# Kernel tuning notes

Hardware: AMD Instinct MI355X
Metric: run time of the kernel (lower is better)

Reference implementation:

```python
import jax, jax.numpy as jnp
import numpy as np

L, B, T = 512, 4096, 25

def setup_inputs() -> dict:
    key = jax.random.key(0)
    k = jax.random.split(key, 5)
    return {
        "emissions": jax.random.normal(k[0], (L, B, T), dtype=jnp.float32),
        "tags": jax.random.randint(k[1], (L, B), 0, T),
        "transitions": jax.random.normal(k[2], (T, T), dtype=jnp.float32) * 0.1,
        "start_transitions": jax.random.normal(k[3], (T,), dtype=jnp.float32) * 0.1,
        "end_transitions": jax.random.normal(k[4], (T,), dtype=jnp.float32) * 0.1,
    }


def _crf_nll(emissions, tags, transitions, start_transitions, end_transitions):
    # emissions: [L,B,T], tags: [L,B] int. Full mask (all timesteps valid).
    b = jnp.arange(emissions.shape[1])
    # ---- numerator: score of the gold path ----
    first = start_transitions[tags[0]] + emissions[0, b, tags[0]]  # [B]

    def num_step(carry, inp):
        prev_tags, score = carry
        em_t, tg_t = inp
        score = score + transitions[prev_tags, tg_t] + em_t[b, tg_t]
        return (tg_t, score), None

    (last_tags, numerator), _ = jax.lax.scan(
        num_step, (tags[0], first), (emissions[1:], tags[1:]))
    numerator = numerator + end_transitions[last_tags]
    # ---- denominator: log partition via forward algorithm ----
    alpha0 = start_transitions[None, :] + emissions[0]  # [B,T]

    def fwd_step(alpha, em_t):
        # alpha: [B,T] (prev tag), transitions: [T_prev, T_next]
        nxt = jax.nn.logsumexp(alpha[:, :, None] + transitions[None, :, :], axis=1) + em_t
        return nxt, None

    alpha, _ = jax.lax.scan(fwd_step, alpha0, emissions[1:])
    log_z = jax.nn.logsumexp(alpha + end_transitions[None, :], axis=1)  # [B]
    # reduction='mean' over batch of log-likelihood, negated
    return -jnp.mean(numerator - log_z)


def _crf_decode(emissions, transitions, start_transitions, end_transitions):
    # Viterbi over [L,B,T] with full mask.
    b = jnp.arange(emissions.shape[1])
    score0 = start_transitions[None, :] + emissions[0]  # [B,T]

    def vit_step(score, em_t):
        # total: [B, T_prev, T_next]
        total = score[:, :, None] + transitions[None, :, :] + em_t[:, None, :]
        best_prev = jnp.argmax(total, axis=1).astype(jnp.int32)  # [B,T]
        return jnp.max(total, axis=1), best_prev

    score, history = jax.lax.scan(vit_step, score0, emissions[1:])  # history [L-1,B,T]
    last_tag = jnp.argmax(score + end_transitions[None, :], axis=1).astype(jnp.int32)  # [B]

    def back_step(nxt_tag, hist_t):
        prev_tag = hist_t[b, nxt_tag]  # [B]
        return prev_tag, prev_tag

    _, prev_tags = jax.lax.scan(back_step, last_tag, history, reverse=True)  # [L-1,B]
    return jnp.concatenate([prev_tags, last_tag[None, :]], axis=0)  # [L,B]


def reference(emissions, tags, transitions, start_transitions, end_transitions):
    nll = _crf_nll(emissions, tags, transitions, start_transitions, end_transitions)
    best_path = _crf_decode(emissions, transitions, start_transitions, end_transitions)
    return nll, best_path
```

## Files before the change

### kernel.cpp

```cpp
#include <hip/hip_runtime.h>

#define TN 25
#define BN 4096
#define LN 512
#define NEG_INF (-__builtin_huge_valf())

__device__ __forceinline__ float gmax32(float x) {
  x = fmaxf(x, __int_as_float(__builtin_amdgcn_ds_swizzle(__float_as_int(x), 0x041F)));
  x = fmaxf(x, __int_as_float(__builtin_amdgcn_ds_swizzle(__float_as_int(x), 0x081F)));
  x = fmaxf(x, __int_as_float(__builtin_amdgcn_ds_swizzle(__float_as_int(x), 0x101F)));
  x = fmaxf(x, __int_as_float(__builtin_amdgcn_ds_swizzle(__float_as_int(x), 0x201F)));
  x = fmaxf(x, __int_as_float(__builtin_amdgcn_ds_swizzle(__float_as_int(x), 0x401F)));
  return x;
}
__device__ __forceinline__ float gsum32(float x) {
  x = x + __int_as_float(__builtin_amdgcn_ds_swizzle(__float_as_int(x), 0x041F));
  x = x + __int_as_float(__builtin_amdgcn_ds_swizzle(__float_as_int(x), 0x081F));
  x = x + __int_as_float(__builtin_amdgcn_ds_swizzle(__float_as_int(x), 0x101F));
  x = x + __int_as_float(__builtin_amdgcn_ds_swizzle(__float_as_int(x), 0x201F));
  x = x + __int_as_float(__builtin_amdgcn_ds_swizzle(__float_as_int(x), 0x401F));
  return x;
}

template <int P>
__device__ __forceinline__ void vit_cand(int sci, const float (&tc)[TN], float em,
                                         float (&v)[TN]) {
  v[P] = (__int_as_float(__builtin_amdgcn_ds_swizzle(sci, (P << 5))) + tc[P]) + em;
  if constexpr (P + 1 < TN) vit_cand<P + 1>(sci, tc, em, v);
}

template <int P>
__device__ __forceinline__ void fwd_acc(int eai, const float (&ec)[TN], float& s0, float& s1) {
  float ep = __int_as_float(__builtin_amdgcn_ds_swizzle(eai, (P << 5)));
  if constexpr ((P & 1) == 0) { s0 = fmaf(ep, ec[P], s0); } else { s1 = fmaf(ep, ec[P], s1); }
  if constexpr (P + 1 < TN) fwd_acc<P + 1>(eai, ec, s0, s1);
}

__global__ __launch_bounds__(512, 4) void crf_main(
    const float* __restrict__ emis, const int* __restrict__ tags,
    const float* __restrict__ trans, const float* __restrict__ startT,
    const float* __restrict__ endT, float* __restrict__ nll_out,
    unsigned char* __restrict__ hist, unsigned char* __restrict__ mmap,
    int* __restrict__ lastTagOut) {
  __shared__ float ltr[TN * TN];
  const int tid = threadIdx.x;
  for (int i = tid; i < TN * TN; i += 512) ltr[i] = trans[i];
  __syncthreads();

  const int j = tid & 31;
  const int grp = tid >> 5;
  const int b = blockIdx.x * 8 + (grp & 7);
  const bool act = (j < TN);
  const int jj = act ? j : 0;
  const float endv = act ? endT[j] : NEG_INF;
  const float* emp = emis + (size_t)b * TN;
  const float em0 = act ? emp[j] : 0.0f;
  const float startv = act ? startT[j] : NEG_INF;

  if (grp < 8) {
    float tc[TN];
#pragma unroll
    for (int p = 0; p < TN; ++p) tc[p] = ltr[p * TN + jj];

    float score = startv + em0;
    int M = j;
    const int bp_base = (tid & 32) << 2;
    unsigned char* hp = hist + ((size_t)BN + b) * 32 + j;

#pragma unroll 1
    for (int t = 1; t < LN; ++t) {
      emp += (size_t)BN * TN;
      float em = act ? emp[j] : 0.0f;

      float v[TN];
      vit_cand<0>(__float_as_int(score), tc, em, v);

      int ix[TN];
#pragma unroll
      for (int p = 0; p < TN; ++p) ix[p] = p;
#pragma unroll
      for (int s = 1; s < TN; s <<= 1) {
#pragma unroll
        for (int i = 0; i + s < TN; i += 2 * s) {
          bool g = v[i + s] > v[i];
          v[i] = g ? v[i + s] : v[i];
          ix[i] = g ? ix[i + s] : ix[i];
        }
      }
      score = v[0];
      int barg = ix[0];

      if (act) *hp = (unsigned char)barg;
      hp += (size_t)BN * 32;

      M = __builtin_amdgcn_ds_bpermute(bp_base + (barg << 2), M);
      if ((t & 31) == 0) {
        int c = (t >> 5) - 1;
        if (act) mmap[((size_t)c * BN + b) * 32 + j] = (unsigned char)M;
        M = j;
      }
    }
    if (act) mmap[((size_t)15 * BN + b) * 32 + j] = (unsigned char)M;

    float vv = score + endv;
    float mv = gmax32(vv);
    unsigned long long bal = __ballot(vv == mv);
    unsigned int gb = (unsigned int)(bal >> (tid & 32));
    int lt = __ffs(gb) - 1;
    if (j == 0) lastTagOut[b] = lt;
  } else {
    float ec[TN];
#pragma unroll
    for (int p = 0; p < TN; ++p) ec[p] = __expf(ltr[p * TN + jj]);

    int tag = tags[b];
    float alpha = startv + em0;
    float num_acc = (j == tag) ? alpha : 0.0f;
    int ptag = tag;

#pragma unroll 1
    for (int t = 1; t < LN; ++t) {
      emp += (size_t)BN * TN;
      float em = act ? emp[j] : 0.0f;
      int tg = tags[(size_t)t * BN + b];

      float mA = __int_as_float(__builtin_amdgcn_ds_swizzle(__float_as_int(alpha), 0x0000));
      float ea = __expf(alpha - mA);

      float s0 = 0.0f, s1 = 0.0f;
      fwd_acc<0>(__float_as_int(ea), ec, s0, s1);
      alpha = act ? (__logf(s0 + s1) + mA + em) : NEG_INF;

      float trc = ltr[ptag * TN + jj];
      num_acc += (j == tg) ? (trc + em) : 0.0f;
      ptag = tg;
    }

    num_acc += (j == ptag) ? endv : 0.0f;
    float numerator = gsum32(num_acc);

    float va = alpha + endv;
    float m2 = gmax32(va);
    float ssum = gsum32(__expf(va - m2));
    float logZ = __logf(ssum) + m2;

    if (j == 0) atomicAdd(nll_out, (logZ - numerator) * (1.0f / BN));
  }
}

__global__ void crf_bstate(const unsigned char* __restrict__ mmap,
                           const int* __restrict__ lastTag,
                           int* __restrict__ estate) {
  int b = blockIdx.x * 256 + threadIdx.x;
  if (b >= BN) return;
  int s = lastTag[b];
  estate[15 * BN + b] = s;
#pragma unroll
  for (int c = 15; c >= 1; --c) {
    s = mmap[((size_t)c * BN + b) * 32 + s];
    estate[(c - 1) * BN + b] = s;
  }
}

__global__ void crf_backtrack(const unsigned char* __restrict__ hist,
                              const int* __restrict__ estate,
                              float* __restrict__ path) {
  int b = blockIdx.x * 256 + threadIdx.x;
  int c = blockIdx.y;
  int s = estate[c * BN + b];
  int te = (c == 15) ? (LN - 1) : 32 * (c + 1);
  for (int t = te; t > 32 * c; --t) {
    path[(size_t)t * BN + b] = (float)s;
    s = hist[((size_t)t * BN + b) * 32 + s];
  }
  if (c == 0) path[b] = (float)s;
}

extern "C" void kernel_launch(void* const* d_in, const int* in_sizes, int n_in,
                              void* d_out, int out_size, void* d_ws, size_t ws_size,
                              hipStream_t stream) {
  const float* emis   = (const float*)d_in[0];
  const int*   tags   = (const int*)d_in[1];
  const float* trans  = (const float*)d_in[2];
  const float* startT = (const float*)d_in[3];
  const float* endT   = (const float*)d_in[4];
  float* out = (float*)d_out;

  unsigned char* hist = (unsigned char*)d_ws;
  unsigned char* mmap = hist + (size_t)LN * BN * 32;
  int* lastTag = (int*)(mmap + (size_t)16 * BN * 32);
  int* estate  = lastTag + BN;

  hipMemsetAsync(d_out, 0, sizeof(float), stream);

  crf_main<<<dim3(BN / 8), 512, 0, stream>>>(emis, tags, trans, startT, endT,
                                             out, hist, mmap, lastTag);
  crf_bstate<<<dim3(BN / 256), 256, 0, stream>>>(mmap, lastTag, estate);
  crf_backtrack<<<dim3(BN / 256, 16), 256, 0, stream>>>(hist, estate, out + 1);
}
```

Baseline: 678.2 us.

## Split each CRF batch row across a full wave with LDS-broadcast recurrences

```diff
diff --git a/kernel.cpp b/kernel.cpp
--- a/kernel.cpp
+++ b/kernel.cpp
@@ -5,66 +5,73 @@
 #define LN 512
 #define NEG_INF (-__builtin_huge_valf())
 
+#define SWZF(x, imm) __int_as_float(__builtin_amdgcn_ds_swizzle(__float_as_int(x), (imm)))
+#define SWZI(x, imm) __builtin_amdgcn_ds_swizzle((x), (imm))
+
 __device__ __forceinline__ float gmax32(float x) {
-  x = fmaxf(x, __int_as_float(__builtin_amdgcn_ds_swizzle(__float_as_int(x), 0x041F)));
-  x = fmaxf(x, __int_as_float(__builtin_amdgcn_ds_swizzle(__float_as_int(x), 0x081F)));
-  x = fmaxf(x, __int_as_float(__builtin_amdgcn_ds_swizzle(__float_as_int(x), 0x101F)));
-  x = fmaxf(x, __int_as_float(__builtin_amdgcn_ds_swizzle(__float_as_int(x), 0x201F)));
-  x = fmaxf(x, __int_as_float(__builtin_amdgcn_ds_swizzle(__float_as_int(x), 0x401F)));
+  x = fmaxf(x, SWZF(x, 0x041F));
+  x = fmaxf(x, SWZF(x, 0x081F));
+  x = fmaxf(x, SWZF(x, 0x101F));
+  x = fmaxf(x, SWZF(x, 0x201F));
+  x = fmaxf(x, SWZF(x, 0x401F));
   return x;
 }
 __device__ __forceinline__ float gsum32(float x) {
-  x = x + __int_as_float(__builtin_amdgcn_ds_swizzle(__float_as_int(x), 0x041F));
-  x = x + __int_as_float(__builtin_amdgcn_ds_swizzle(__float_as_int(x), 0x081F));
-  x = x + __int_as_float(__builtin_amdgcn_ds_swizzle(__float_as_int(x), 0x101F));
-  x = x + __int_as_float(__builtin_amdgcn_ds_swizzle(__float_as_int(x), 0x201F));
-  x = x + __int_as_float(__builtin_amdgcn_ds_swizzle(__float_as_int(x), 0x401F));
+  x = x + SWZF(x, 0x041F);
+  x = x + SWZF(x, 0x081F);
+  x = x + SWZF(x, 0x101F);
+  x = x + SWZF(x, 0x201F);
+  x = x + SWZF(x, 0x401F);
   return x;
 }
 
-template <int P>
-__device__ __forceinline__ void vit_cand(int sci, const float (&tc)[TN], float em,
-                                         float (&v)[TN]) {
-  v[P] = (__int_as_float(__builtin_amdgcn_ds_swizzle(sci, (P << 5))) + tc[P]) + em;
-  if constexpr (P + 1 < TN) vit_cand<P + 1>(sci, tc, em, v);
-}
-
-template <int P>
-__device__ __forceinline__ void fwd_acc(int eai, const float (&ec)[TN], float& s0, float& s1) {
-  float ep = __int_as_float(__builtin_amdgcn_ds_swizzle(eai, (P << 5)));
-  if constexpr ((P & 1) == 0) { s0 = fmaf(ep, ec[P], s0); } else { s1 = fmaf(ep, ec[P], s1); }
-  if constexpr (P + 1 < TN) fwd_acc<P + 1>(eai, ec, s0, s1);
-}
-
-__global__ __launch_bounds__(512, 4) void crf_main(
+__global__ __launch_bounds__(512, 8) void crf_main(
     const float* __restrict__ emis, const int* __restrict__ tags,
     const float* __restrict__ trans, const float* __restrict__ startT,
     const float* __restrict__ endT, float* __restrict__ nll_out,
     unsigned char* __restrict__ hist, unsigned char* __restrict__ mmap,
     int* __restrict__ lastTagOut) {
   __shared__ float ltr[TN * TN];
+  __shared__ float ltrT[TN][36];
+  __shared__ float sv[8][32];
+
   const int tid = threadIdx.x;
-  for (int i = tid; i < TN * TN; i += 512) ltr[i] = trans[i];
+  for (int i = tid; i < TN * TN; i += 512) {
+    float v = trans[i];
+    ltr[i] = v;
+    ltrT[i % TN][i / TN] = v;
+  }
   __syncthreads();
 
-  const int j = tid & 31;
-  const int grp = tid >> 5;
-  const int b = blockIdx.x * 8 + (grp & 7);
+  const int wave = tid >> 6;
+  const int lane = tid & 63;
+  const int h = lane >> 5;
+  const int j = lane & 31;
+  const int b = blockIdx.x * 4 + (wave & 3);
   const bool act = (j < TN);
   const int jj = act ? j : 0;
+  const int pbase = h ? 12 : 0;
   const float endv = act ? endT[j] : NEG_INF;
   const float* emp = emis + (size_t)b * TN;
   const float em0 = act ? emp[j] : 0.0f;
   const float startv = act ? startT[j] : NEG_INF;
-
-  if (grp < 8) {
-    float tc[TN];
-#pragma unroll
-    for (int p = 0; p < TN; ++p) tc[p] = ltr[p * TN + jj];
-
+  float* svp = sv[wave];
+
+  float tcv[13];
+  {
+    const float4 a = *(const float4*)&ltrT[jj][pbase];
+    const float4 c = *(const float4*)&ltrT[jj][pbase + 4];
+    const float4 d = *(const float4*)&ltrT[jj][pbase + 8];
+    tcv[0] = a.x; tcv[1] = a.y; tcv[2] = a.z; tcv[3] = a.w;
+    tcv[4] = c.x; tcv[5] = c.y; tcv[6] = c.z; tcv[7] = c.w;
+    tcv[8] = d.x; tcv[9] = d.y; tcv[10] = d.z; tcv[11] = d.w;
+    tcv[12] = h ? ltrT[jj][24] : NEG_INF;
+  }
+
+  if (wave < 4) {
     float score = startv + em0;
+    if (h == 0 && act) svp[j] = score;
     int M = j;
-    const int bp_base = (tid & 32) << 2;
     unsigned char* hp = hist + ((size_t)BN + b) * 32 + j;
 
 #pragma unroll 1
@@ -72,51 +79,67 @@
       emp += (size_t)BN * TN;
       float em = act ? emp[j] : 0.0f;
 
-      float v[TN];
-      vit_cand<0>(__float_as_int(score), tc, em, v);
-
-      int ix[TN];
-#pragma unroll
-      for (int p = 0; p < TN; ++p) ix[p] = p;
-#pragma unroll
-      for (int s = 1; s < TN; s <<= 1) {
-#pragma unroll
-        for (int i = 0; i + s < TN; i += 2 * s) {
-          bool g = v[i + s] > v[i];
-          v[i] = g ? v[i + s] : v[i];
-          ix[i] = g ? ix[i + s] : ix[i];
+      const float4 a = *(const float4*)&svp[pbase];
+      const float4 c = *(const float4*)&svp[pbase + 4];
+      const float4 d = *(const float4*)&svp[pbase + 8];
+      const float sp12 = svp[pbase + 12];
+
+      float v[13]; int ix[13];
+      v[0] = (a.x + tcv[0]) + em;  v[1] = (a.y + tcv[1]) + em;
+      v[2] = (a.z + tcv[2]) + em;  v[3] = (a.w + tcv[3]) + em;
+      v[4] = (c.x + tcv[4]) + em;  v[5] = (c.y + tcv[5]) + em;
+      v[6] = (c.z + tcv[6]) + em;  v[7] = (c.w + tcv[7]) + em;
+      v[8] = (d.x + tcv[8]) + em;  v[9] = (d.y + tcv[9]) + em;
+      v[10] = (d.z + tcv[10]) + em; v[11] = (d.w + tcv[11]) + em;
+      v[12] = (sp12 + tcv[12]) + em;
+#pragma unroll
+      for (int k = 0; k < 13; ++k) ix[k] = pbase + k;
+
+#pragma unroll
+      for (int s = 1; s < 13; s <<= 1) {
+#pragma unroll
+        for (int i2 = 0; i2 + s < 13; i2 += 2 * s) {
+          bool g = v[i2 + s] > v[i2];
+          v[i2] = g ? v[i2 + s] : v[i2];
+          ix[i2] = g ? ix[i2 + s] : ix[i2];
         }
       }
-      score = v[0];
-      int barg = ix[0];
-
-      if (act) *hp = (unsigned char)barg;
+
+      float vo = SWZF(v[0], 0x401F);
+      int go = SWZI(ix[0], 0x401F);
+      float vh1 = h ? v[0] : vo, vh0 = h ? vo : v[0];
+      int gh1 = h ? ix[0] : go, gh0 = h ? go : ix[0];
+      bool better = vh1 > vh0;
+      score = better ? vh1 : vh0;
+      int barg = better ? gh1 : gh0;
+
+      if (h == 0 && act) svp[j] = score;
+      if (h == 0 && act) *hp = (unsigned char)barg;
       hp += (size_t)BN * 32;
 
-      M = __builtin_amdgcn_ds_bpermute(bp_base + (barg << 2), M);
+      M = __builtin_amdgcn_ds_bpermute((barg & 31) << 2, M);
       if ((t & 31) == 0) {
-        int c = (t >> 5) - 1;
-        if (act) mmap[((size_t)c * BN + b) * 32 + j] = (unsigned char)M;
+        int c2 = (t >> 5) - 1;
+        if (h == 0 && act) mmap[((size_t)c2 * BN + b) * 32 + j] = (unsigned char)M;
         M = j;
       }
     }
-    if (act) mmap[((size_t)15 * BN + b) * 32 + j] = (unsigned char)M;
+    if (h == 0 && act) mmap[((size_t)15 * BN + b) * 32 + j] = (unsigned char)M;
 
     float vv = score + endv;
     float mv = gmax32(vv);
     unsigned long long bal = __ballot(vv == mv);
-    unsigned int gb = (unsigned int)(bal >> (tid & 32));
+    unsigned int gb = (unsigned int)(bal >> (lane & 32));
     int lt = __ffs(gb) - 1;
-    if (j == 0) lastTagOut[b] = lt;
+    if (lane == 0) lastTagOut[b] = lt;
   } else {
-    float ec[TN];
-#pragma unroll
-    for (int p = 0; p < TN; ++p) ec[p] = __expf(ltr[p * TN + jj]);
-
-    int tag = tags[b];
+    float ecv[13];
+#pragma unroll
+    for (int k = 0; k < 13; ++k) ecv[k] = __expf(tcv[k]);
+
+    int ptag = tags[b];
     float alpha = startv + em0;
-    float num_acc = (j == tag) ? alpha : 0.0f;
-    int ptag = tag;
+    float num_acc = (act && j == ptag) ? alpha : 0.0f;
 
 #pragma unroll 1
     for (int t = 1; t < LN; ++t) {
@@ -124,19 +147,34 @@
       float em = act ? emp[j] : 0.0f;
       int tg = tags[(size_t)t * BN + b];
 
-      float mA = __int_as_float(__builtin_amdgcn_ds_swizzle(__float_as_int(alpha), 0x0000));
+      float mA = SWZF(alpha, 0x0000);
       float ea = __expf(alpha - mA);
-
-      float s0 = 0.0f, s1 = 0.0f;
-      fwd_acc<0>(__float_as_int(ea), ec, s0, s1);
-      alpha = act ? (__logf(s0 + s1) + mA + em) : NEG_INF;
+      if (h == 0 && act) svp[j] = ea;
+
+      const float4 a = *(const float4*)&svp[pbase];
+      const float4 c = *(const float4*)&svp[pbase + 4];
+      const float4 d = *(const float4*)&svp[pbase + 8];
+      const float ep12 = svp[pbase + 12];
+
+      float s0 = a.x * ecv[0];
+      float s1 = a.y * ecv[1];
+      s0 = fmaf(a.z, ecv[2], s0);  s1 = fmaf(a.w, ecv[3], s1);
+      s0 = fmaf(c.x, ecv[4], s0);  s1 = fmaf(c.y, ecv[5], s1);
+      s0 = fmaf(c.z, ecv[6], s0);  s1 = fmaf(c.w, ecv[7], s1);
+      s0 = fmaf(d.x, ecv[8], s0);  s1 = fmaf(d.y, ecv[9], s1);
+      s0 = fmaf(d.z, ecv[10], s0); s1 = fmaf(d.w, ecv[11], s1);
+      s0 = fmaf(ep12, ecv[12], s0);
+      float s = s0 + s1;
+      float tot = s + SWZF(s, 0x401F);
+
+      alpha = act ? (__logf(tot) + mA + em) : NEG_INF;
 
       float trc = ltr[ptag * TN + jj];
-      num_acc += (j == tg) ? (trc + em) : 0.0f;
+      num_acc += (act && j == tg) ? (trc + em) : 0.0f;
       ptag = tg;
     }
 
-    num_acc += (j == ptag) ? endv : 0.0f;
+    num_acc += (act && j == ptag) ? endv : 0.0f;
     float numerator = gsum32(num_acc);
 
     float va = alpha + endv;
@@ -144,7 +182,7 @@
     float ssum = gsum32(__expf(va - m2));
     float logZ = __logf(ssum) + m2;
 
-    if (j == 0) atomicAdd(nll_out, (logZ - numerator) * (1.0f / BN));
+    if (lane == 0) atomicAdd(nll_out, (logZ - numerator) * (1.0f / BN));
   }
 }
 
@@ -193,7 +231,7 @@
 
   hipMemsetAsync(d_out, 0, sizeof(float), stream);
 
-  crf_main<<<dim3(BN / 8), 512, 0, stream>>>(emis, tags, trans, startT, endT,
+  crf_main<<<dim3(BN / 4), 512, 0, stream>>>(emis, tags, trans, startT, endT,
                                              out, hist, mmap, lastTag);
   crf_bstate<<<dim3(BN / 256), 256, 0, stream>>>(mmap, lastTag, estate);
   crf_backtrack<<<dim3(BN / 256, 16), 256, 0, stream>>>(hist, estate, out + 1);
```

Result: no change. 678.5 us (+0.1%).

## Broadcast states via LDS vector reads and split Viterbi/forward into separate blocks

Applied to the files above, without the earlier changes.

```diff
diff --git a/kernel.cpp b/kernel.cpp
--- a/kernel.cpp
+++ b/kernel.cpp
@@ -3,66 +3,89 @@
 #define TN 25
 #define BN 4096
 #define LN 512
+#define NVB 512
 #define NEG_INF (-__builtin_huge_valf())
 
+#define SWZF(x, imm) __int_as_float(__builtin_amdgcn_ds_swizzle(__float_as_int(x), (imm)))
+
 __device__ __forceinline__ float gmax32(float x) {
-  x = fmaxf(x, __int_as_float(__builtin_amdgcn_ds_swizzle(__float_as_int(x), 0x041F)));
-  x = fmaxf(x, __int_as_float(__builtin_amdgcn_ds_swizzle(__float_as_int(x), 0x081F)));
-  x = fmaxf(x, __int_as_float(__builtin_amdgcn_ds_swizzle(__float_as_int(x), 0x101F)));
-  x = fmaxf(x, __int_as_float(__builtin_amdgcn_ds_swizzle(__float_as_int(x), 0x201F)));
-  x = fmaxf(x, __int_as_float(__builtin_amdgcn_ds_swizzle(__float_as_int(x), 0x401F)));
+  x = fmaxf(x, SWZF(x, 0x041F));
+  x = fmaxf(x, SWZF(x, 0x081F));
+  x = fmaxf(x, SWZF(x, 0x101F));
+  x = fmaxf(x, SWZF(x, 0x201F));
+  x = fmaxf(x, SWZF(x, 0x401F));
   return x;
 }
 __device__ __forceinline__ float gsum32(float x) {
-  x = x + __int_as_float(__builtin_amdgcn_ds_swizzle(__float_as_int(x), 0x041F));
-  x = x + __int_as_float(__builtin_amdgcn_ds_swizzle(__float_as_int(x), 0x081F));
-  x = x + __int_as_float(__builtin_amdgcn_ds_swizzle(__float_as_int(x), 0x101F));
-  x = x + __int_as_float(__builtin_amdgcn_ds_swizzle(__float_as_int(x), 0x201F));
-  x = x + __int_as_float(__builtin_amdgcn_ds_swizzle(__float_as_int(x), 0x401F));
+  x = x + SWZF(x, 0x041F);
+  x = x + SWZF(x, 0x081F);
+  x = x + SWZF(x, 0x101F);
+  x = x + SWZF(x, 0x201F);
+  x = x + SWZF(x, 0x401F);
   return x;
 }
 
-template <int P>
-__device__ __forceinline__ void vit_cand(int sci, const float (&tc)[TN], float em,
-                                         float (&v)[TN]) {
-  v[P] = (__int_as_float(__builtin_amdgcn_ds_swizzle(sci, (P << 5))) + tc[P]) + em;
-  if constexpr (P + 1 < TN) vit_cand<P + 1>(sci, tc, em, v);
-}
-
-template <int P>
-__device__ __forceinline__ void fwd_acc(int eai, const float (&ec)[TN], float& s0, float& s1) {
-  float ep = __int_as_float(__builtin_amdgcn_ds_swizzle(eai, (P << 5)));
-  if constexpr ((P & 1) == 0) { s0 = fmaf(ep, ec[P], s0); } else { s1 = fmaf(ep, ec[P], s1); }
-  if constexpr (P + 1 < TN) fwd_acc<P + 1>(eai, ec, s0, s1);
-}
-
-__global__ __launch_bounds__(512, 4) void crf_main(
+__device__ __forceinline__ void read_vec25(const float* __restrict__ p, float (&o)[TN]) {
+  const float4 q0 = *(const float4*)(p + 0);
+  const float4 q1 = *(const float4*)(p + 4);
+  const float4 q2 = *(const float4*)(p + 8);
+  const float4 q3 = *(const float4*)(p + 12);
+  const float4 q4 = *(const float4*)(p + 16);
+  const float4 q5 = *(const float4*)(p + 20);
+  o[0]=q0.x;  o[1]=q0.y;  o[2]=q0.z;  o[3]=q0.w;
+  o[4]=q1.x;  o[5]=q1.y;  o[6]=q1.z;  o[7]=q1.w;
+  o[8]=q2.x;  o[9]=q2.y;  o[10]=q2.z; o[11]=q2.w;
+  o[12]=q3.x; o[13]=q3.y; o[14]=q3.z; o[15]=q3.w;
+  o[16]=q4.x; o[17]=q4.y; o[18]=q4.z; o[19]=q4.w;
+  o[20]=q5.x; o[21]=q5.y; o[22]=q5.z; o[23]=q5.w;
+  o[24]=p[24];
+}
+
+__device__ __forceinline__ void merge3(float va, int ia, float vb, int ib, float vc, int ic,
+                                       float& mo, int& io) {
+  float m = fmaxf(fmaxf(va, vb), vc);
+  io = (m == va) ? ia : ((m == vb) ? ib : ic);
+  mo = m;
+}
+
+__global__ __launch_bounds__(256, 8) void crf_main(
     const float* __restrict__ emis, const int* __restrict__ tags,
     const float* __restrict__ trans, const float* __restrict__ startT,
     const float* __restrict__ endT, float* __restrict__ nll_out,
     unsigned char* __restrict__ hist, unsigned char* __restrict__ mmap,
     int* __restrict__ lastTagOut) {
   __shared__ float ltr[TN * TN];
+  __shared__ float ltrT[TN][28];
+  __shared__ float eltrT[TN][28];
+  __shared__ float sv[8][32];
+
   const int tid = threadIdx.x;
-  for (int i = tid; i < TN * TN; i += 512) ltr[i] = trans[i];
+  for (int i = tid; i < TN * TN; i += 256) {
+    float v = trans[i];
+    ltr[i] = v;
+    ltrT[i % TN][i / TN] = v;
+    eltrT[i % TN][i / TN] = __expf(v);
+  }
   __syncthreads();
 
   const int j = tid & 31;
   const int grp = tid >> 5;
-  const int b = blockIdx.x * 8 + (grp & 7);
   const bool act = (j < TN);
   const int jj = act ? j : 0;
   const float endv = act ? endT[j] : NEG_INF;
-  const float* emp = emis + (size_t)b * TN;
-  const float em0 = act ? emp[j] : 0.0f;
-  const float startv = act ? startT[j] : NEG_INF;
-
-  if (grp < 8) {
+  float* svp = sv[grp];
+
+  if (blockIdx.x < NVB) {
+    const int b = blockIdx.x * 8 + grp;
+    const float* emp = emis + (size_t)b * TN;
+    const float em0 = act ? emp[j] : 0.0f;
+    const float startv = act ? startT[j] : NEG_INF;
+
     float tc[TN];
-#pragma unroll
-    for (int p = 0; p < TN; ++p) tc[p] = ltr[p * TN + jj];
+    read_vec25(&ltrT[jj][0], tc);
 
     float score = startv + em0;
+    if (act) svp[j] = score;
     int M = j;
     const int bp_base = (tid & 32) << 2;
     unsigned char* hp = hist + ((size_t)BN + b) * 32 + j;
@@ -72,31 +95,35 @@
       emp += (size_t)BN * TN;
       float em = act ? emp[j] : 0.0f;
 
+      float sp[TN];
+      read_vec25(svp, sp);
+
       float v[TN];
-      vit_cand<0>(__float_as_int(score), tc, em, v);
-
-      int ix[TN];
-#pragma unroll
-      for (int p = 0; p < TN; ++p) ix[p] = p;
-#pragma unroll
-      for (int s = 1; s < TN; s <<= 1) {
-#pragma unroll
-        for (int i = 0; i + s < TN; i += 2 * s) {
-          bool g = v[i + s] > v[i];
-          v[i] = g ? v[i + s] : v[i];
-          ix[i] = g ? ix[i + s] : ix[i];
-        }
-      }
-      score = v[0];
-      int barg = ix[0];
-
+#pragma unroll
+      for (int p = 0; p < TN; ++p) v[p] = sp[p] + tc[p];
+
+      float w[9]; int wi[9];
+#pragma unroll
+      for (int g = 0; g < 8; ++g)
+        merge3(v[3*g], 3*g, v[3*g+1], 3*g+1, v[3*g+2], 3*g+2, w[g], wi[g]);
+      w[8] = v[24]; wi[8] = 24;
+      float u0, u1, u2; int x0, x1, x2;
+      merge3(w[0], wi[0], w[1], wi[1], w[2], wi[2], u0, x0);
+      merge3(w[3], wi[3], w[4], wi[4], w[5], wi[5], u1, x1);
+      merge3(w[6], wi[6], w[7], wi[7], w[8], wi[8], u2, x2);
+      float best; int barg;
+      merge3(u0, x0, u1, x1, u2, x2, best, barg);
+
+      score = best + em;
+
+      if (act) svp[j] = score;
       if (act) *hp = (unsigned char)barg;
       hp += (size_t)BN * 32;
 
       M = __builtin_amdgcn_ds_bpermute(bp_base + (barg << 2), M);
       if ((t & 31) == 0) {
-        int c = (t >> 5) - 1;
-        if (act) mmap[((size_t)c * BN + b) * 32 + j] = (unsigned char)M;
+        int c2 = (t >> 5) - 1;
+        if (act) mmap[((size_t)c2 * BN + b) * 32 + j] = (unsigned char)M;
         M = j;
       }
     }
@@ -109,14 +136,17 @@
     int lt = __ffs(gb) - 1;
     if (j == 0) lastTagOut[b] = lt;
   } else {
+    const int b = (blockIdx.x - NVB) * 8 + grp;
+    const float* emp = emis + (size_t)b * TN;
+    const float em0 = act ? emp[j] : 0.0f;
+    const float startv = act ? startT[j] : NEG_INF;
+
     float ec[TN];
-#pragma unroll
-    for (int p = 0; p < TN; ++p) ec[p] = __expf(ltr[p * TN + jj]);
-
-    int tag = tags[b];
+    read_vec25(&eltrT[jj][0], ec);
+
+    int ptag = tags[b];
     float alpha = startv + em0;
-    float num_acc = (j == tag) ? alpha : 0.0f;
-    int ptag = tag;
+    float num_acc = (act && j == ptag) ? alpha : 0.0f;
 
 #pragma unroll 1
     for (int t = 1; t < LN; ++t) {
@@ -124,19 +154,27 @@
       float em = act ? emp[j] : 0.0f;
       int tg = tags[(size_t)t * BN + b];
 
-      float mA = __int_as_float(__builtin_amdgcn_ds_swizzle(__float_as_int(alpha), 0x0000));
+      float mA = SWZF(alpha, 0x0000);
       float ea = __expf(alpha - mA);
-
-      float s0 = 0.0f, s1 = 0.0f;
-      fwd_acc<0>(__float_as_int(ea), ec, s0, s1);
+      if (act) svp[j] = ea;
+
+      float ep[TN];
+      read_vec25(svp, ep);
+
+      float s0 = ep[0] * ec[0];
+      float s1 = ep[1] * ec[1];
+#pragma unroll
+      for (int p = 2; p < TN; p += 2) s0 = fmaf(ep[p], ec[p], s0);
+#pragma unroll
+      for (int p = 3; p < TN; p += 2) s1 = fmaf(ep[p], ec[p], s1);
       alpha = act ? (__logf(s0 + s1) + mA + em) : NEG_INF;
 
       float trc = ltr[ptag * TN + jj];
-      num_acc += (j == tg) ? (trc + em) : 0.0f;
+      num_acc += (act && j == tg) ? (trc + em) : 0.0f;
       ptag = tg;
     }
 
-    num_acc += (j == ptag) ? endv : 0.0f;
+    num_acc += (act && j == ptag) ? endv : 0.0f;
     float numerator = gsum32(num_acc);
 
     float va = alpha + endv;
@@ -193,8 +231,8 @@
 
   hipMemsetAsync(d_out, 0, sizeof(float), stream);
 
-  crf_main<<<dim3(BN / 8), 512, 0, stream>>>(emis, tags, trans, startT, endT,
-                                             out, hist, mmap, lastTag);
+  crf_main<<<dim3(2 * NVB), 256, 0, stream>>>(emis, tags, trans, startT, endT,
+                                              out, hist, mmap, lastTag);
   crf_bstate<<<dim3(BN / 256), 256, 0, stream>>>(mmap, lastTag, estate);
   crf_backtrack<<<dim3(BN / 256, 16), 256, 0, stream>>>(hist, estate, out + 1);
 }
```

After: 555.1 us. -18.1%, faster.
